# Kernel optimization log

Hardware: AMD Instinct MI355X
Metric: run time of the kernel (lower is better)

The kernel has to match this reference:

```python
import jax, jax.numpy as jnp
import numpy as np

MAX_ITERS = 256  # matches init_kwargs max_iters


def setup_inputs() -> dict:
    key = jax.random.key(0)
    k1, k2 = jax.random.split(key)
    H = W = 4096
    # classic Mandelbrot viewing window
    c_real = jax.random.uniform(k1, (H, W), jnp.float32, -2.0, 0.5)
    c_imag = jax.random.uniform(k2, (H, W), jnp.float32, -1.25, 1.25)
    return {"c_real": c_real, "c_imag": c_imag}


def reference(c_real, c_imag):
    # z starts at c (NOT zero), as in the torch module
    zr0 = c_real
    zi0 = c_imag
    active0 = jnp.ones(c_real.shape, dtype=bool)
    counts0 = jnp.full(c_real.shape, float(MAX_ITERS), dtype=c_real.dtype)

    def body(step, state):
        zr, zi, active, counts = state
        escaped_now = active & (zr * zr + zi * zi >= 4.0)
        counts = jnp.where(escaped_now, step.astype(counts.dtype), counts)
        active = active & ~escaped_now
        # torch loop only updates z for step < max_iters
        do_update = active & (step < MAX_ITERS)
        next_real = zr * zr - zi * zi + c_real
        next_imag = 2.0 * zr * zi + c_imag
        zr = jnp.where(do_update, next_real, zr)
        zi = jnp.where(do_update, next_imag, zi)
        return (zr, zi, active, counts)

    _, _, _, counts = jax.lax.fori_loop(
        0, MAX_ITERS + 1, body, (zr0, zi0, active0, counts0)
    )
    return counts
```

## Files before the change

kernel.cpp:

```cpp
#include <hip/hip_runtime.h>


#define MAX_ITERS 256

__device__ __forceinline__ float mul32(float a, float b) {
    float d; asm("v_mul_f32 %0, %1, %2" : "=v"(d) : "v"(a), "v"(b)); return d;
}
__device__ __forceinline__ float add32(float a, float b) {
    float d; asm("v_add_f32 %0, %1, %2" : "=v"(d) : "v"(a), "v"(b)); return d;
}
__device__ __forceinline__ float fma32(float a, float b, float c) {
    float d; asm("v_fma_f32 %0, %1, %2, %3" : "=v"(d) : "v"(a), "v"(b), "v"(c)); return d;
}
__device__ __forceinline__ float fma32_negc(float a, float b, float c) {
    float d; asm("v_fma_f32 %0, %1, %2, -%3" : "=v"(d) : "v"(a), "v"(b), "v"(c)); return d;
}

__device__ __forceinline__ void iter_checks(float cr, float ci,
                                            float& zr, float& zi,
                                            float& act, float& cnt, int nchecks)
{
    #pragma unroll 8
    for (int s = 0; s < nchecks; ++s) {
        const float zi2 = mul32(zi, zi);
        const float mag = fma32(zr, zr, zi2);
        act = (mag < 4.0f) ? act : 0.0f;
        cnt = cnt + act;
        const float t   = fma32_negc(zr, zr, zi2);
        const float nr  = add32(t, cr);
        const float t2  = add32(zr, zr);
        zi = fma32(t2, zi, ci);
        zr = nr;
    }
}

__device__ __forceinline__ int lane_id() {
    return __builtin_amdgcn_mbcnt_hi(~0u, __builtin_amdgcn_mbcnt_lo(~0u, 0));
}

__global__ void zero_ctrs(unsigned char* ws) {
    if (threadIdx.x < 256)
        *(unsigned*)(ws + (size_t)(threadIdx.x >> 2) * 64u
                        + (size_t)(threadIdx.x & 3) * 4u) = 0u;
}

__global__ __launch_bounds__(256) void mandel_stage_a(
    const float* __restrict__ c_real, const float* __restrict__ c_imag,
    float* __restrict__ out, unsigned char* __restrict__ ws,
    unsigned seg_cap, int n)
{
    int i = blockIdx.x * blockDim.x + threadIdx.x;
    if (i >= n) return;
    const float cr = c_real[i];
    const float ci = c_imag[i];

    const float xq = cr - 0.25f;
    const float q  = xq * xq + ci * ci;
    const bool in_card = (q * (q + xq) - 0.25f * ci * ci) < -1e-3f;
    const float xb = cr + 1.0f;
    const bool in_bulb = (xb * xb + ci * ci) < (0.0625f - 1e-3f);
    const bool shortcut = in_card | in_bulb;

    float zr = cr, zi = ci, act = 1.0f, cnt = 0.0f;
    iter_checks(cr, ci, zr, zi, act, cnt, 16);

    const bool surv = (!shortcut) && (act != 0.0f);

    const unsigned long long m = __ballot(surv);
    if (m != 0ull) {
        const int lane = lane_id();
        const int leader = (int)__ffsll((unsigned long long)m) - 1;
        const int seg = blockIdx.x & 63;
        unsigned* ctr = (unsigned*)(ws + (size_t)seg * 64u);
        unsigned base = 0u;
        if (lane == leader) base = atomicAdd(ctr, (unsigned)__popcll(m));
        base = (unsigned)__shfl((int)base, leader, 64);
        if (surv) {
            const unsigned rank = (unsigned)__popcll(m & ((1ull << lane) - 1ull));
            const unsigned slot = base + rank;
            if (slot < seg_cap) {
                float4* q1f = (float4*)(ws + 4096);
                int*    q1i = (int*)(ws + 4096 + (size_t)seg_cap * 64u * 16u);
                const size_t p = (size_t)seg * seg_cap + slot;
                q1f[p] = make_float4(zr, zi, cr, ci);
                q1i[p] = i;
                return;
            }
            iter_checks(cr, ci, zr, zi, act, cnt, 240);
            out[i] = cnt;
            return;
        }
    }
    out[i] = shortcut ? 256.0f : cnt;
}

template <int NCHECKS, int START, bool HAS_DST>
__global__ __launch_bounds__(256) void mandel_strip(
    float* __restrict__ out, unsigned char* __restrict__ ws,
    const float4* __restrict__ srcF, const int* __restrict__ srcI,
    float4* __restrict__ dstF, int* __restrict__ dstI,
    int src_ctr, int dst_ctr, unsigned seg_cap, int blocks_per_seg)
{
    const int seg = (int)(blockIdx.x & 63u);
    const int grp = (int)(blockIdx.x >> 6);
    const unsigned cnt_s = *(const unsigned*)(ws + (size_t)seg * 64u
                                                 + (size_t)src_ctr * 4u);
    const unsigned nq = (cnt_s < seg_cap) ? cnt_s : seg_cap;
    const unsigned stride = (unsigned)blocks_per_seg * 256u;
    const int lane = lane_id();

    for (unsigned j = (unsigned)grp * 256u + threadIdx.x; j < nq; j += stride) {
        const size_t p = (size_t)seg * seg_cap + j;
        const float4 rec = srcF[p];
        const int idx = srcI[p];
        float zr = rec.x, zi = rec.y;
        const float cr = rec.z, ci = rec.w;
        float act = 1.0f, cnt = (float)START;
        iter_checks(cr, ci, zr, zi, act, cnt, NCHECKS);

        if (HAS_DST) {
            const bool surv = (act != 0.0f);
            const unsigned long long m = __ballot(surv);
            if (m != 0ull) {
                const int leader = (int)__ffsll((unsigned long long)m) - 1;
                unsigned* ctr = (unsigned*)(ws + (size_t)seg * 64u
                                               + (size_t)dst_ctr * 4u);
                unsigned base = 0u;
                if (lane == leader) base = atomicAdd(ctr, (unsigned)__popcll(m));
                base = (unsigned)__shfl((int)base, leader, 64);
                if (surv) {
                    const unsigned rank =
                        (unsigned)__popcll(m & ((1ull << lane) - 1ull));
                    const unsigned slot = base + rank;
                    if (slot < seg_cap) {
                        const size_t sp = (size_t)seg * seg_cap + slot;
                        dstF[sp] = make_float4(zr, zi, cr, ci);
                        dstI[sp] = idx;
                        continue;
                    }
                    iter_checks(cr, ci, zr, zi, act, cnt,
                                256 - START - NCHECKS);
                    out[idx] = cnt;
                    continue;
                }
            }
            out[idx] = cnt;
        } else {
            out[idx] = cnt;
        }
    }
}

__global__ __launch_bounds__(256) void mandel_stage_b_fixed(
    float* __restrict__ out, const unsigned char* __restrict__ ws,
    unsigned seg_cap, int blocks_per_seg)
{
    const int seg = (int)(blockIdx.x & 63u);
    const int grp = (int)(blockIdx.x >> 6);
    const unsigned cnt_s = *(const unsigned*)(ws + (size_t)seg * 64u);
    const unsigned nq = (cnt_s < seg_cap) ? cnt_s : seg_cap;
    const float4* q1f = (const float4*)(ws + 4096);
    const int*    q1i = (const int*)(ws + 4096 + (size_t)seg_cap * 64u * 16u);
    const unsigned stride = (unsigned)blocks_per_seg * 256u;
    for (unsigned j = (unsigned)grp * 256u + threadIdx.x; j < nq; j += stride) {
        const size_t p = (size_t)seg * seg_cap + j;
        const float4 rec = q1f[p];
        const int idx = q1i[p];
        float zr = rec.x, zi = rec.y;
        const float cr = rec.z, ci = rec.w;
        float act = 1.0f, cnt = 16.0f;
        iter_checks(cr, ci, zr, zi, act, cnt, 240);
        out[idx] = cnt;
    }
}

__global__ __launch_bounds__(256) void mandel_mono(
    const float* __restrict__ c_real, const float* __restrict__ c_imag,
    float* __restrict__ out, int n)
{
    int i = blockIdx.x * blockDim.x + threadIdx.x;
    if (i >= n) return;
    const float cr = c_real[i], ci = c_imag[i];
    float zr = cr, zi = ci, act = 1.0f, cnt = 0.0f;
    iter_checks(cr, ci, zr, zi, act, cnt, MAX_ITERS);
    out[i] = cnt;
}

extern "C" void kernel_launch(void* const* d_in, const int* in_sizes, int n_in,
                              void* d_out, int out_size, void* d_ws, size_t ws_size,
                              hipStream_t stream)
{
    const float* c_real = (const float*)d_in[0];
    const float* c_imag = (const float*)d_in[1];
    float* out = (float*)d_out;
    const int n = in_sizes[0];
    const int block = 256;
    const int gridA = (n + block - 1) / block;

    unsigned char* ws = (unsigned char*)d_ws;
    const size_t avail = (ws_size > 4096) ? (ws_size - 4096) : 0;
    const unsigned seg_cap1 = (unsigned)(avail / (64u * 20u));
    const unsigned seg_cap2 = (unsigned)(avail / (64u * 20u * 2u));

    if (seg_cap1 < 1024u) {
        mandel_mono<<<gridA, block, 0, stream>>>(c_real, c_imag, out, n);
        return;
    }

    zero_ctrs<<<1, 256, 0, stream>>>(ws);

    if (seg_cap2 >= 33000u) {
        const unsigned sc = seg_cap2;
        float4* q0f = (float4*)(ws + 4096);
        int*    q0i = (int*)(ws + 4096 + (size_t)sc * 64u * 16u);
        float4* q1f = (float4*)(ws + 4096 + (size_t)sc * 64u * 20u);
        int*    q1i = (int*)(ws + 4096 + (size_t)sc * 64u * 20u
                                       + (size_t)sc * 64u * 16u);

        mandel_stage_a<<<gridA, block, 0, stream>>>(c_real, c_imag, out, ws,
                                                    sc, n);
        mandel_strip<40, 16, true><<<64 * 128, block, 0, stream>>>(
            out, ws, q0f, q0i, q1f, q1i, 0, 1, sc, 128);
        mandel_strip<80, 56, true><<<64 * 64, block, 0, stream>>>(
            out, ws, q1f, q1i, q0f, q0i, 1, 2, sc, 64);
        mandel_strip<120, 136, false><<<64 * 64, block, 0, stream>>>(
            out, ws, q0f, q0i, (float4*)nullptr, (int*)nullptr, 2, 0, sc, 64);
        return;
    }

    mandel_stage_a<<<gridA, block, 0, stream>>>(c_real, c_imag, out, ws,
                                                seg_cap1, n);
    const int blocks_per_seg = 256;
    mandel_stage_b_fixed<<<64 * blocks_per_seg, block, 0, stream>>>(
        out, ws, seg_cap1, blocks_per_seg);
}
```

Baseline: 252.6 us.

## Process two pixels per thread using packed FP32 instructions

Rewrites stage A and the strip kernels so each thread iterates two points at once with v_pk_mul/add/fma_f32, and halves the grid sizes to match. The aim is to double arithmetic throughput per instruction on the compute-bound escape loop. Compaction uses two ballots per wave, and the per-point compare and select stay scalar. The risks are higher register pressure, and divergence because a pair keeps running until both of its points escape.

Measured after the change: 234.8 us. 1.08x faster.

```diff
diff --git a/kernel.cpp b/kernel.cpp
--- a/kernel.cpp
+++ b/kernel.cpp
@@ -2,6 +2,8 @@
 
 
 #define MAX_ITERS 256
+
+typedef __attribute__((ext_vector_type(2))) float f32x2;
 
 __device__ __forceinline__ float mul32(float a, float b) {
     float d; asm("v_mul_f32 %0, %1, %2" : "=v"(d) : "v"(a), "v"(b)); return d;
@@ -34,38 +36,228 @@
     }
 }
 
+__device__ __forceinline__ f32x2 pk_mul(f32x2 a, f32x2 b) {
+    f32x2 d; asm("v_pk_mul_f32 %0, %1, %2" : "=v"(d) : "v"(a), "v"(b)); return d;
+}
+__device__ __forceinline__ f32x2 pk_add(f32x2 a, f32x2 b) {
+    f32x2 d; asm("v_pk_add_f32 %0, %1, %2" : "=v"(d) : "v"(a), "v"(b)); return d;
+}
+__device__ __forceinline__ f32x2 pk_fma(f32x2 a, f32x2 b, f32x2 c) {
+    f32x2 d; asm("v_pk_fma_f32 %0, %1, %2, %3" : "=v"(d) : "v"(a), "v"(b), "v"(c)); return d;
+}
+
+__device__ __forceinline__ void iter_checks_pk(const f32x2 cr, const f32x2 ci,
+                                               f32x2& zr, f32x2& zi,
+                                               f32x2& act, f32x2& cnt,
+                                               int nchecks)
+{
+    #pragma unroll 8
+    for (int s = 0; s < nchecks; ++s) {
+        const f32x2 zi2  = pk_mul(zi, zi);
+        const f32x2 mag  = pk_fma(zr, zr, zi2);
+        const f32x2 mzi2 = -zi2;
+        const f32x2 t    = pk_fma(zr, zr, mzi2);
+        const f32x2 nr   = pk_add(t, cr);
+        const f32x2 t2   = pk_add(zr, zr);
+        const f32x2 nzi  = pk_fma(t2, zi, ci);
+        act.x = (mag.x < 4.0f) ? act.x : 0.0f;
+        act.y = (mag.y < 4.0f) ? act.y : 0.0f;
+        cnt = pk_add(cnt, act);
+        zr = nr; zi = nzi;
+    }
+}
+
 __device__ __forceinline__ int lane_id() {
     return __builtin_amdgcn_mbcnt_hi(~0u, __builtin_amdgcn_mbcnt_lo(~0u, 0));
 }
 
-__global__ void zero_ctrs(unsigned char* ws) {
-    if (threadIdx.x < 256)
-        *(unsigned*)(ws + (size_t)(threadIdx.x >> 2) * 64u
-                        + (size_t)(threadIdx.x & 3) * 4u) = 0u;
-}
-
-__global__ __launch_bounds__(256) void mandel_stage_a(
-    const float* __restrict__ c_real, const float* __restrict__ c_imag,
-    float* __restrict__ out, unsigned char* __restrict__ ws,
-    unsigned seg_cap, int n)
-{
-    int i = blockIdx.x * blockDim.x + threadIdx.x;
-    if (i >= n) return;
-    const float cr = c_real[i];
-    const float ci = c_imag[i];
-
+__device__ __forceinline__ bool in_shortcut(float cr, float ci) {
     const float xq = cr - 0.25f;
     const float q  = xq * xq + ci * ci;
     const bool in_card = (q * (q + xq) - 0.25f * ci * ci) < -1e-3f;
     const float xb = cr + 1.0f;
     const bool in_bulb = (xb * xb + ci * ci) < (0.0625f - 1e-3f);
-    const bool shortcut = in_card | in_bulb;
+    return in_card | in_bulb;
+}
+
+__global__ void zero_ctrs(unsigned char* ws) {
+    if (threadIdx.x < 256)
+        *(unsigned*)(ws + (size_t)(threadIdx.x >> 2) * 64u
+                        + (size_t)(threadIdx.x & 3) * 4u) = 0u;
+}
+
+__global__ __launch_bounds__(256) void mandel_stage_a_pk(
+    const float* __restrict__ c_real, const float* __restrict__ c_imag,
+    float* __restrict__ out, unsigned char* __restrict__ ws,
+    unsigned seg_cap, int n)
+{
+    const int tp = blockIdx.x * blockDim.x + threadIdx.x;
+    const int p0 = tp << 1;
+    if (p0 >= n) return;
+    const bool has1 = (p0 + 1) < n;
+
+    f32x2 cr, ci;
+    if (has1) {
+        cr = *(const f32x2*)(c_real + p0);
+        ci = *(const f32x2*)(c_imag + p0);
+    } else {
+        cr.x = c_real[p0]; cr.y = 0.0f;
+        ci.x = c_imag[p0]; ci.y = 0.0f;
+    }
+    const bool sc0 = in_shortcut(cr.x, ci.x);
+    const bool sc1 = in_shortcut(cr.y, ci.y);
+
+    f32x2 zr = cr, zi = ci;
+    f32x2 act; act.x = 1.0f; act.y = has1 ? 1.0f : 0.0f;
+    f32x2 cnt = {0.0f, 0.0f};
+    iter_checks_pk(cr, ci, zr, zi, act, cnt, 16);
+
+    const bool s0 = (!sc0) && (act.x != 0.0f);
+    const bool s1 = has1 && (!sc1) && (act.y != 0.0f);
+
+    const unsigned long long m0 = __ballot(s0);
+    const unsigned long long m1 = __ballot(s1);
+    if ((m0 | m1) != 0ull) {
+        const int lane = lane_id();
+        const int leader = (int)__ffsll(m0 | m1) - 1;
+        const int seg = blockIdx.x & 63;
+        unsigned* ctr = (unsigned*)(ws + (size_t)seg * 64u);
+        unsigned base = 0u;
+        if (lane == leader)
+            base = atomicAdd(ctr, (unsigned)(__popcll(m0) + __popcll(m1)));
+        base = (unsigned)__shfl((int)base, leader, 64);
+        float4* qf = (float4*)(ws + 4096);
+        int*    qi = (int*)(ws + 4096 + (size_t)seg_cap * 64u * 16u);
+        if (s0) {
+            const unsigned slot = base +
+                (unsigned)__popcll(m0 & ((1ull << lane) - 1ull));
+            if (slot < seg_cap) {
+                const size_t p = (size_t)seg * seg_cap + slot;
+                qf[p] = make_float4(zr.x, zi.x, cr.x, ci.x);
+                qi[p] = p0;
+            } else {
+                float zrs = zr.x, zis = zi.x, as = 1.0f, cs = cnt.x;
+                iter_checks(cr.x, ci.x, zrs, zis, as, cs, 240);
+                out[p0] = cs;
+            }
+        }
+        if (s1) {
+            const unsigned slot = base + (unsigned)__popcll(m0) +
+                (unsigned)__popcll(m1 & ((1ull << lane) - 1ull));
+            if (slot < seg_cap) {
+                const size_t p = (size_t)seg * seg_cap + slot;
+                qf[p] = make_float4(zr.y, zi.y, cr.y, ci.y);
+                qi[p] = p0 + 1;
+            } else {
+                float zrs = zr.y, zis = zi.y, as = 1.0f, cs = cnt.y;
+                iter_checks(cr.y, ci.y, zrs, zis, as, cs, 240);
+                out[p0 + 1] = cs;
+            }
+        }
+    }
+    if (!s0) out[p0] = sc0 ? 256.0f : cnt.x;
+    if (has1 && !s1) out[p0 + 1] = sc1 ? 256.0f : cnt.y;
+}
+
+template <int NCHECKS, int START, bool HAS_DST>
+__global__ __launch_bounds__(256) void mandel_strip_pk(
+    float* __restrict__ out, unsigned char* __restrict__ ws,
+    const float4* __restrict__ srcF, const int* __restrict__ srcI,
+    float4* __restrict__ dstF, int* __restrict__ dstI,
+    int src_ctr, int dst_ctr, unsigned seg_cap, int blocks_per_seg)
+{
+    const int seg = (int)(blockIdx.x & 63u);
+    const int grp = (int)(blockIdx.x >> 6);
+    const unsigned cnt_s = *(const unsigned*)(ws + (size_t)seg * 64u
+                                                 + (size_t)src_ctr * 4u);
+    const unsigned nq = (cnt_s < seg_cap) ? cnt_s : seg_cap;
+    const unsigned half = (nq + 1u) >> 1;
+    const unsigned stride = (unsigned)blocks_per_seg * 256u;
+    const int lane = lane_id();
+    const size_t segbase = (size_t)seg * seg_cap;
+
+    for (unsigned k = (unsigned)grp * 256u + threadIdx.x; k < half; k += stride) {
+        const unsigned r1 = k + half;
+        const bool v1 = (r1 < nq);
+        const float4 rec0 = srcF[segbase + k];
+        const float4 rec1 = v1 ? srcF[segbase + r1] : rec0;
+        const int idx0 = srcI[segbase + k];
+        const int idx1 = v1 ? srcI[segbase + r1] : -1;
+        f32x2 zr; zr.x = rec0.x; zr.y = rec1.x;
+        f32x2 zi; zi.x = rec0.y; zi.y = rec1.y;
+        f32x2 cr; cr.x = rec0.z; cr.y = rec1.z;
+        f32x2 ci; ci.x = rec0.w; ci.y = rec1.w;
+        f32x2 act; act.x = 1.0f; act.y = v1 ? 1.0f : 0.0f;
+        f32x2 cnt = {(float)START, (float)START};
+        iter_checks_pk(cr, ci, zr, zi, act, cnt, NCHECKS);
+        const bool s0 = (act.x != 0.0f);
+        const bool s1 = (act.y != 0.0f);
+
+        if (HAS_DST) {
+            const unsigned long long m0 = __ballot(s0);
+            const unsigned long long m1 = __ballot(s1);
+            if ((m0 | m1) != 0ull) {
+                const int leader = (int)__ffsll(m0 | m1) - 1;
+                unsigned* ctr = (unsigned*)(ws + (size_t)seg * 64u
+                                               + (size_t)dst_ctr * 4u);
+                unsigned base = 0u;
+                if (lane == leader)
+                    base = atomicAdd(ctr,
+                        (unsigned)(__popcll(m0) + __popcll(m1)));
+                base = (unsigned)__shfl((int)base, leader, 64);
+                if (s0) {
+                    const unsigned slot = base +
+                        (unsigned)__popcll(m0 & ((1ull << lane) - 1ull));
+                    if (slot < seg_cap) {
+                        const size_t sp = segbase + slot;
+                        dstF[sp] = make_float4(zr.x, zi.x, cr.x, ci.x);
+                        dstI[sp] = idx0;
+                    } else {
+                        float zrs = zr.x, zis = zi.x, as = 1.0f, cs = cnt.x;
+                        iter_checks(cr.x, ci.x, zrs, zis, as, cs,
+                                    256 - START - NCHECKS);
+                        out[idx0] = cs;
+                    }
+                }
+                if (s1) {
+                    const unsigned slot = base + (unsigned)__popcll(m0) +
+                        (unsigned)__popcll(m1 & ((1ull << lane) - 1ull));
+                    if (slot < seg_cap) {
+                        const size_t sp = segbase + slot;
+                        dstF[sp] = make_float4(zr.y, zi.y, cr.y, ci.y);
+                        dstI[sp] = idx1;
+                    } else {
+                        float zrs = zr.y, zis = zi.y, as = 1.0f, cs = cnt.y;
+                        iter_checks(cr.y, ci.y, zrs, zis, as, cs,
+                                    256 - START - NCHECKS);
+                        out[idx1] = cs;
+                    }
+                }
+            }
+            if (!s0) out[idx0] = cnt.x;
+            if (v1 && !s1) out[idx1] = cnt.y;
+        } else {
+            out[idx0] = cnt.x;
+            if (v1) out[idx1] = cnt.y;
+        }
+    }
+}
+
+__global__ __launch_bounds__(256) void mandel_stage_a(
+    const float* __restrict__ c_real, const float* __restrict__ c_imag,
+    float* __restrict__ out, unsigned char* __restrict__ ws,
+    unsigned seg_cap, int n)
+{
+    int i = blockIdx.x * blockDim.x + threadIdx.x;
+    if (i >= n) return;
+    const float cr = c_real[i];
+    const float ci = c_imag[i];
+    const bool shortcut = in_shortcut(cr, ci);
 
     float zr = cr, zi = ci, act = 1.0f, cnt = 0.0f;
     iter_checks(cr, ci, zr, zi, act, cnt, 16);
 
     const bool surv = (!shortcut) && (act != 0.0f);
-
     const unsigned long long m = __ballot(surv);
     if (m != 0ull) {
         const int lane = lane_id();
@@ -94,63 +286,6 @@
     out[i] = shortcut ? 256.0f : cnt;
 }
 
-template <int NCHECKS, int START, bool HAS_DST>
-__global__ __launch_bounds__(256) void mandel_strip(
-    float* __restrict__ out, unsigned char* __restrict__ ws,
-    const float4* __restrict__ srcF, const int* __restrict__ srcI,
-    float4* __restrict__ dstF, int* __restrict__ dstI,
-    int src_ctr, int dst_ctr, unsigned seg_cap, int blocks_per_seg)
-{
-    const int seg = (int)(blockIdx.x & 63u);
-    const int grp = (int)(blockIdx.x >> 6);
-    const unsigned cnt_s = *(const unsigned*)(ws + (size_t)seg * 64u
-                                                 + (size_t)src_ctr * 4u);
-    const unsigned nq = (cnt_s < seg_cap) ? cnt_s : seg_cap;
-    const unsigned stride = (unsigned)blocks_per_seg * 256u;
-    const int lane = lane_id();
-
-    for (unsigned j = (unsigned)grp * 256u + threadIdx.x; j < nq; j += stride) {
-        const size_t p = (size_t)seg * seg_cap + j;
-        const float4 rec = srcF[p];
-        const int idx = srcI[p];
-        float zr = rec.x, zi = rec.y;
-        const float cr = rec.z, ci = rec.w;
-        float act = 1.0f, cnt = (float)START;
-        iter_checks(cr, ci, zr, zi, act, cnt, NCHECKS);
-
-        if (HAS_DST) {
-            const bool surv = (act != 0.0f);
-            const unsigned long long m = __ballot(surv);
-            if (m != 0ull) {
-                const int leader = (int)__ffsll((unsigned long long)m) - 1;
-                unsigned* ctr = (unsigned*)(ws + (size_t)seg * 64u
-                                               + (size_t)dst_ctr * 4u);
-                unsigned base = 0u;
-                if (lane == leader) base = atomicAdd(ctr, (unsigned)__popcll(m));
-                base = (unsigned)__shfl((int)base, leader, 64);
-                if (surv) {
-                    const unsigned rank =
-                        (unsigned)__popcll(m & ((1ull << lane) - 1ull));
-                    const unsigned slot = base + rank;
-                    if (slot < seg_cap) {
-                        const size_t sp = (size_t)seg * seg_cap + slot;
-                        dstF[sp] = make_float4(zr, zi, cr, ci);
-                        dstI[sp] = idx;
-                        continue;
-                    }
-                    iter_checks(cr, ci, zr, zi, act, cnt,
-                                256 - START - NCHECKS);
-                    out[idx] = cnt;
-                    continue;
-                }
-            }
-            out[idx] = cnt;
-        } else {
-            out[idx] = cnt;
-        }
-    }
-}
-
 __global__ __launch_bounds__(256) void mandel_stage_b_fixed(
     float* __restrict__ out, const unsigned char* __restrict__ ws,
     unsigned seg_cap, int blocks_per_seg)
@@ -195,7 +330,6 @@
     float* out = (float*)d_out;
     const int n = in_sizes[0];
     const int block = 256;
-    const int gridA = (n + block - 1) / block;
 
     unsigned char* ws = (unsigned char*)d_ws;
     const size_t avail = (ws_size > 4096) ? (ws_size - 4096) : 0;
@@ -203,6 +337,7 @@
     const unsigned seg_cap2 = (unsigned)(avail / (64u * 20u * 2u));
 
     if (seg_cap1 < 1024u) {
+        const int gridA = (n + block - 1) / block;
         mandel_mono<<<gridA, block, 0, stream>>>(c_real, c_imag, out, n);
         return;
     }
@@ -217,17 +352,20 @@
         int*    q1i = (int*)(ws + 4096 + (size_t)sc * 64u * 20u
                                        + (size_t)sc * 64u * 16u);
 
-        mandel_stage_a<<<gridA, block, 0, stream>>>(c_real, c_imag, out, ws,
-                                                    sc, n);
-        mandel_strip<40, 16, true><<<64 * 128, block, 0, stream>>>(
-            out, ws, q0f, q0i, q1f, q1i, 0, 1, sc, 128);
-        mandel_strip<80, 56, true><<<64 * 64, block, 0, stream>>>(
-            out, ws, q1f, q1i, q0f, q0i, 1, 2, sc, 64);
-        mandel_strip<120, 136, false><<<64 * 64, block, 0, stream>>>(
-            out, ws, q0f, q0i, (float4*)nullptr, (int*)nullptr, 2, 0, sc, 64);
+        const int npairs = (n + 1) / 2;
+        const int gridA = (npairs + block - 1) / block;
+        mandel_stage_a_pk<<<gridA, block, 0, stream>>>(c_real, c_imag, out,
+                                                       ws, sc, n);
+        mandel_strip_pk<40, 16, true><<<64 * 64, block, 0, stream>>>(
+            out, ws, q0f, q0i, q1f, q1i, 0, 1, sc, 64);
+        mandel_strip_pk<80, 56, true><<<64 * 32, block, 0, stream>>>(
+            out, ws, q1f, q1i, q0f, q0i, 1, 2, sc, 32);
+        mandel_strip_pk<120, 136, false><<<64 * 32, block, 0, stream>>>(
+            out, ws, q0f, q0i, (float4*)nullptr, (int*)nullptr, 2, 0, sc, 32);
         return;
     }
 
+    const int gridA = (n + block - 1) / block;
     mandel_stage_a<<<gridA, block, 0, stream>>>(c_real, c_imag, out, ws,
                                                 seg_cap1, n);
     const int blocks_per_seg = 256;
```
